# Optimization experiments

Hardware: AMD Instinct MI355X
Metric: run time of the kernel (lower is better)

## Reference

```python
import jax, jax.numpy as jnp
import numpy as np

EPS_RMS = 1e-8
EPS_Q = 1e-5


def rms_norm(x, scale):
    # full RMSNorm (p=-1): rms = ||x||_2 / sqrt(d); y = scale * x / (rms + eps)
    d = x.shape[-1]
    norm = jnp.linalg.norm(x, axis=-1, keepdims=True)
    rms = norm * (d ** -0.5)
    return scale * (x / (rms + EPS_RMS))


def activation_quant(x):
    # per-token int8 abs-max quant
    s = 127.0 / jnp.clip(jnp.max(jnp.abs(x), axis=-1, keepdims=True), EPS_Q, None)
    return jnp.clip(jnp.round(x * s), -128, 127) / s


def weight_quant(w):
    # per-tensor ternary abs-mean quant
    s = 1.0 / jnp.clip(jnp.mean(jnp.abs(w)), EPS_Q, None)
    return jnp.clip(jnp.round(w * s), -1, 1) / s


def bit_linear(x, w, scale):
    x_q = activation_quant(rms_norm(x, scale))  # forward value of STE
    w_q = weight_quant(w)
    return x_q @ w_q.T


def setup_inputs() -> dict:
    key = jax.random.key(0)
    ks = jax.random.split(key, 4)
    B = 65536
    x = jax.random.normal(ks[0], (B, 784), dtype=jnp.float32)
    w1 = jax.random.normal(ks[1], (128, 784), dtype=jnp.float32) * (784 ** -0.5)
    w2 = jax.random.normal(ks[2], (64, 128), dtype=jnp.float32) * (128 ** -0.5)
    w3 = jax.random.normal(ks[3], (10, 64), dtype=jnp.float32) * (64 ** -0.5)
    return {
        'x': x,
        'w1': w1, 'scale1': jnp.ones((784,), jnp.float32),
        'w2': w2, 'scale2': jnp.ones((128,), jnp.float32),
        'w3': w3, 'scale3': jnp.ones((64,), jnp.float32),
    }


def reference(x, w1, scale1, w2, scale2, w3, scale3):
    h = jax.nn.relu(bit_linear(x, w1, scale1))
    h = jax.nn.relu(bit_linear(h, w2, scale2))
    return bit_linear(h, w3, scale3)
```

## Files before the change

kernel.cpp:

```cpp
#include <hip/hip_runtime.h>
#include <stdint.h>


typedef int   ix4 __attribute__((ext_vector_type(4)));
typedef float fx4 __attribute__((ext_vector_type(4)));

#define MFMA_I8(a, b, c) __builtin_amdgcn_mfma_i32_16x16x64_i8((a), (b), (c), 0, 0, 0)

__device__ __forceinline__ void sync_lds() {
  asm volatile("s_waitcnt lgkmcnt(0)" ::: "memory");
  __builtin_amdgcn_s_barrier();
}
__device__ __forceinline__ void wave_lds_fence() {
  asm volatile("s_waitcnt lgkmcnt(0)" ::: "memory");
}

__global__ __launch_bounds__(256) void prep_mean(
    const float* __restrict__ w1, const float* __restrict__ w2,
    const float* __restrict__ w3, double* __restrict__ sums) {
  __shared__ double red[256];
  const int b = blockIdx.x;
  const float* w; int n, nb, bb, which;
  if (b < 240)      { w = w1; n = 128 * 784; nb = 240; bb = b;       which = 0; }
  else if (b < 248) { w = w2; n = 64 * 128;  nb = 8;   bb = b - 240; which = 1; }
  else              { w = w3; n = 10 * 64;   nb = 1;   bb = 0;       which = 2; }
  double s = 0.0;
  for (int i = bb * 256 + (int)threadIdx.x; i < n; i += nb * 256)
    s += (double)fabsf(w[i]);
  red[threadIdx.x] = s;
  __syncthreads();
  for (int off = 128; off > 0; off >>= 1) {
    if ((int)threadIdx.x < off) red[threadIdx.x] += red[threadIdx.x + off];
    __syncthreads();
  }
  if (threadIdx.x == 0) atomicAdd(&sums[which], red[0]);
}

__global__ __launch_bounds__(256) void prep_quant(
    const float* __restrict__ w1, const float* __restrict__ w2,
    const float* __restrict__ w3, const double* __restrict__ sums,
    int8_t* __restrict__ t1, int8_t* __restrict__ t2,
    int8_t* __restrict__ t3p) {
  const int idx = blockIdx.x * 256 + (int)threadIdx.x;
  const float s1 = 1.0f / fmaxf((float)(sums[0] * (1.0 / (128.0 * 784.0))), 1e-5f);
  const float s2 = 1.0f / fmaxf((float)(sums[1] * (1.0 / (64.0 * 128.0))), 1e-5f);
  const float s3 = 1.0f / fmaxf((float)(sums[2] * (1.0 / (10.0 * 64.0))), 1e-5f);
  if (idx < 128 * 832) {
    const int n = idx / 832, k = idx - n * 832;
    float v = 0.f;
    if (k < 784) v = fminf(fmaxf(rintf(w1[n * 784 + k] * s1), -1.f), 1.f);
    t1[idx] = (int8_t)(int)v;
  } else if (idx < 128 * 832 + 64 * 128) {
    const int i = idx - 128 * 832;
    t2[i] = (int8_t)(int)fminf(fmaxf(rintf(w2[i] * s2), -1.f), 1.f);
  } else if (idx < 128 * 832 + 64 * 128 + 16 * 64) {
    const int i = idx - (128 * 832 + 64 * 128);
    const int n = i >> 6, p = i & 63;
    const int ch = (p >> 2) + 16 * (p & 3);
    float v = 0.f;
    if (n < 10) v = fminf(fmaxf(rintf(w3[n * 64 + ch] * s3), -1.f), 1.f);
    t3p[i] = (int8_t)(int)v;
  }
}

__global__ __launch_bounds__(256)
__attribute__((amdgpu_waves_per_eu(2, 4)))
void ffn_l1(
    const float* __restrict__ x,
    const float* __restrict__ sc1, const float* __restrict__ sc2,
    const int8_t* __restrict__ t1, const double* __restrict__ sums,
    int8_t* __restrict__ q2g, float* __restrict__ inv2g, int numTiles) {
  __shared__ int8_t q1[16 * 848];
  __shared__ float  h1[16 * 132];
  __shared__ float  inv1[16];

  const int tid = threadIdx.x;
  const int l   = tid & 63;
  const int wv  = tid >> 6;
  const int g   = l >> 4;
  const int sl  = l & 15;
  const int token = wv * 4 + g;

  const float m1 = fmaxf((float)(sums[0] * (1.0 / (128.0 * 784.0))), 1e-5f);

  if (tid < 192) {
    const int t = tid / 12, c = tid - (tid / 12) * 12;
    *reinterpret_cast<unsigned*>(&q1[t * 848 + 784 + c * 4]) = 0u;
  }

  fx4 xv[13];
  int tile = blockIdx.x;
  if (tile < numTiles) {
    const float* rowp = x + (size_t)(tile * 16 + token) * 784;
#pragma unroll
    for (int c = 0; c < 12; ++c)
      xv[c] = *reinterpret_cast<const fx4*>(rowp + (sl + 16 * c) * 4);
    if (sl < 4) xv[12] = *reinterpret_cast<const fx4*>(rowp + (sl + 192) * 4);
  }

  for (; tile < numTiles; tile += (int)gridDim.x) {
    float ss = 0.f, am = 0.f;
#pragma unroll
    for (int c = 0; c < 12; ++c) {
      fx4 v = xv[c];
      fx4 s4 = *reinterpret_cast<const fx4*>(sc1 + (sl + 16 * c) * 4);
      ss += v[0] * v[0] + v[1] * v[1] + v[2] * v[2] + v[3] * v[3];
      am = fmaxf(am, fmaxf(fmaxf(fabsf(v[0] * s4[0]), fabsf(v[1] * s4[1])),
                           fmaxf(fabsf(v[2] * s4[2]), fabsf(v[3] * s4[3]))));
    }
    if (sl < 4) {
      fx4 v = xv[12];
      fx4 s4 = *reinterpret_cast<const fx4*>(sc1 + (sl + 192) * 4);
      ss += v[0] * v[0] + v[1] * v[1] + v[2] * v[2] + v[3] * v[3];
      am = fmaxf(am, fmaxf(fmaxf(fabsf(v[0] * s4[0]), fabsf(v[1] * s4[1])),
                           fmaxf(fabsf(v[2] * s4[2]), fabsf(v[3] * s4[3]))));
    }
#pragma unroll
    for (int m = 1; m < 16; m <<= 1) {
      ss += __shfl_xor(ss, m, 64);
      am = fmaxf(am, __shfl_xor(am, m, 64));
    }
    const float denom = sqrtf(ss) * (1.0f / 28.0f) + 1e-8f;
    const float invd  = 1.0f / denom;
    const float cl    = fmaxf(am * invd, 1e-5f);
    const float gq    = (127.0f / cl) * invd;
    if (sl == 0) inv1[token] = cl * (1.0f / 127.0f);

#pragma unroll
    for (int c = 0; c < 12; ++c) {
      fx4 v = xv[c];
      fx4 s4 = *reinterpret_cast<const fx4*>(sc1 + (sl + 16 * c) * 4);
      int q0 = (int)fminf(fmaxf(rintf(v[0] * s4[0] * gq), -128.f), 127.f);
      int q1i = (int)fminf(fmaxf(rintf(v[1] * s4[1] * gq), -128.f), 127.f);
      int q2i = (int)fminf(fmaxf(rintf(v[2] * s4[2] * gq), -128.f), 127.f);
      int q3i = (int)fminf(fmaxf(rintf(v[3] * s4[3] * gq), -128.f), 127.f);
      unsigned p = (unsigned)(q0 & 255) | ((unsigned)(q1i & 255) << 8) |
                   ((unsigned)(q2i & 255) << 16) | ((unsigned)(q3i & 255) << 24);
      *reinterpret_cast<unsigned*>(&q1[token * 848 + (sl + 16 * c) * 4]) = p;
    }
    if (sl < 4) {
      fx4 v = xv[12];
      fx4 s4 = *reinterpret_cast<const fx4*>(sc1 + (sl + 192) * 4);
      int q0 = (int)fminf(fmaxf(rintf(v[0] * s4[0] * gq), -128.f), 127.f);
      int q1i = (int)fminf(fmaxf(rintf(v[1] * s4[1] * gq), -128.f), 127.f);
      int q2i = (int)fminf(fmaxf(rintf(v[2] * s4[2] * gq), -128.f), 127.f);
      int q3i = (int)fminf(fmaxf(rintf(v[3] * s4[3] * gq), -128.f), 127.f);
      unsigned p = (unsigned)(q0 & 255) | ((unsigned)(q1i & 255) << 8) |
                   ((unsigned)(q2i & 255) << 16) | ((unsigned)(q3i & 255) << 24);
      *reinterpret_cast<unsigned*>(&q1[token * 848 + (sl + 192) * 4]) = p;
    }

    {
      const int ntile = tile + (int)gridDim.x;
      if (ntile < numTiles) {
        const float* rowp = x + (size_t)(ntile * 16 + token) * 784;
#pragma unroll
        for (int c = 0; c < 12; ++c)
          xv[c] = *reinterpret_cast<const fx4*>(rowp + (sl + 16 * c) * 4);
        if (sl < 4) xv[12] = *reinterpret_cast<const fx4*>(rowp + (sl + 192) * 4);
      }
    }

    sync_lds();

    ix4 acc0 = {0, 0, 0, 0}, acc1 = {0, 0, 0, 0};
    {
      const int8_t* b0p = t1 + (wv * 32 + sl) * 832;
      const int8_t* b1p = b0p + 16 * 832;
#pragma unroll 4
      for (int kk = 0; kk < 13; ++kk) {
        const int k0 = kk * 64 + g * 16;
        ix4 a  = *reinterpret_cast<const ix4*>(&q1[sl * 848 + k0]);
        ix4 b0 = *reinterpret_cast<const ix4*>(b0p + k0);
        ix4 b1 = *reinterpret_cast<const ix4*>(b1p + k0);
        acc0 = MFMA_I8(a, b0, acc0);
        acc1 = MFMA_I8(a, b1, acc1);
      }
    }
#pragma unroll
    for (int r = 0; r < 4; ++r) {
      const int tr = g * 4 + r;
      const float s = inv1[tr] * m1;
      h1[tr * 132 + wv * 32 + sl]      = fmaxf((float)acc0[r] * s, 0.f);
      h1[tr * 132 + wv * 32 + 16 + sl] = fmaxf((float)acc1[r] * s, 0.f);
    }
    sync_lds();

    {
      fx4 v0 = *reinterpret_cast<const fx4*>(&h1[token * 132 + sl * 4]);
      fx4 v1 = *reinterpret_cast<const fx4*>(&h1[token * 132 + 64 + sl * 4]);
      fx4 s0 = *reinterpret_cast<const fx4*>(sc2 + sl * 4);
      fx4 s1 = *reinterpret_cast<const fx4*>(sc2 + 64 + sl * 4);
      float ss2 = v0[0]*v0[0] + v0[1]*v0[1] + v0[2]*v0[2] + v0[3]*v0[3]
                + v1[0]*v1[0] + v1[1]*v1[1] + v1[2]*v1[2] + v1[3]*v1[3];
      float am2 = fmaxf(fmaxf(fmaxf(fabsf(v0[0]*s0[0]), fabsf(v0[1]*s0[1])),
                              fmaxf(fabsf(v0[2]*s0[2]), fabsf(v0[3]*s0[3]))),
                        fmaxf(fmaxf(fabsf(v1[0]*s1[0]), fabsf(v1[1]*s1[1])),
                              fmaxf(fabsf(v1[2]*s1[2]), fabsf(v1[3]*s1[3]))));
#pragma unroll
      for (int m = 1; m < 16; m <<= 1) {
        ss2 += __shfl_xor(ss2, m, 64);
        am2 = fmaxf(am2, __shfl_xor(am2, m, 64));
      }
      const float den2 = sqrtf(ss2) * 0.08838834764831845f + 1e-8f;
      const float id2  = 1.0f / den2;
      const float cl2  = fmaxf(am2 * id2, 1e-5f);
      const float gq2  = (127.0f / cl2) * id2;
      const size_t tok = (size_t)tile * 16 + token;
      if (sl == 0) inv2g[tok] = cl2 * (1.0f / 127.0f);
      int a0 = (int)fminf(fmaxf(rintf(v0[0]*s0[0]*gq2), -128.f), 127.f);
      int a1 = (int)fminf(fmaxf(rintf(v0[1]*s0[1]*gq2), -128.f), 127.f);
      int a2 = (int)fminf(fmaxf(rintf(v0[2]*s0[2]*gq2), -128.f), 127.f);
      int a3 = (int)fminf(fmaxf(rintf(v0[3]*s0[3]*gq2), -128.f), 127.f);
      int b0 = (int)fminf(fmaxf(rintf(v1[0]*s1[0]*gq2), -128.f), 127.f);
      int b1 = (int)fminf(fmaxf(rintf(v1[1]*s1[1]*gq2), -128.f), 127.f);
      int b2 = (int)fminf(fmaxf(rintf(v1[2]*s1[2]*gq2), -128.f), 127.f);
      int b3 = (int)fminf(fmaxf(rintf(v1[3]*s1[3]*gq2), -128.f), 127.f);
      unsigned pa = (unsigned)(a0 & 255) | ((unsigned)(a1 & 255) << 8) |
                    ((unsigned)(a2 & 255) << 16) | ((unsigned)(a3 & 255) << 24);
      unsigned pb = (unsigned)(b0 & 255) | ((unsigned)(b1 & 255) << 8) |
                    ((unsigned)(b2 & 255) << 16) | ((unsigned)(b3 & 255) << 24);
      *reinterpret_cast<unsigned*>(q2g + tok * 128 + sl * 4)      = pa;
      *reinterpret_cast<unsigned*>(q2g + tok * 128 + 64 + sl * 4) = pb;
    }
  }
}

__global__ __launch_bounds__(256) void ffn_l23(
    const int8_t* __restrict__ q2g, const float* __restrict__ inv2g,
    const float* __restrict__ sc3,
    const int8_t* __restrict__ t2, const int8_t* __restrict__ t3p,
    const double* __restrict__ sums, float* __restrict__ out) {
  __shared__ int8_t wbuf[4][16 * 64];

  const int tid = threadIdx.x;
  const int l   = tid & 63;
  const int wv  = tid >> 6;
  const int g   = l >> 4;
  const int sl  = l & 15;
  const int wtok0 = (blockIdx.x * 4 + wv) * 16;

  const float m2 = fmaxf((float)(sums[1] * (1.0 / (64.0 * 128.0))), 1e-5f);
  const float m3 = fmaxf((float)(sums[2] * (1.0 / (10.0 * 64.0))), 1e-5f);

  ix4 a0 = *reinterpret_cast<const ix4*>(q2g + (size_t)(wtok0 + sl) * 128 + g * 16);
  ix4 a1 = *reinterpret_cast<const ix4*>(q2g + (size_t)(wtok0 + sl) * 128 + 64 + g * 16);
  fx4 i2 = *reinterpret_cast<const fx4*>(inv2g + wtok0 + 4 * g);

  ix4 acc[4];
#pragma unroll
  for (int nt = 0; nt < 4; ++nt) {
    ix4 c = {0, 0, 0, 0};
    const int8_t* bp = t2 + (nt * 16 + sl) * 128;
    c = MFMA_I8(a0, *reinterpret_cast<const ix4*>(bp + g * 16), c);
    c = MFMA_I8(a1, *reinterpret_cast<const ix4*>(bp + 64 + g * 16), c);
    acc[nt] = c;
  }

  float sc3v[4];
#pragma unroll
  for (int nt = 0; nt < 4; ++nt) sc3v[nt] = sc3[nt * 16 + sl];

  float h2v[4][4];
  float ss3[4] = {0.f, 0.f, 0.f, 0.f}, am3[4] = {0.f, 0.f, 0.f, 0.f};
#pragma unroll
  for (int nt = 0; nt < 4; ++nt)
#pragma unroll
    for (int r = 0; r < 4; ++r) {
      float h = fmaxf((float)acc[nt][r] * i2[r] * m2, 0.f);
      h2v[nt][r] = h;
      ss3[r] += h * h;
      am3[r] = fmaxf(am3[r], fabsf(h * sc3v[nt]));
    }
#pragma unroll
  for (int m = 1; m < 16; m <<= 1) {
#pragma unroll
    for (int r = 0; r < 4; ++r) {
      ss3[r] += __shfl_xor(ss3[r], m, 64);
      am3[r] = fmaxf(am3[r], __shfl_xor(am3[r], m, 64));
    }
  }
  float gq3[4], i3[4];
#pragma unroll
  for (int r = 0; r < 4; ++r) {
    const float den3 = sqrtf(ss3[r]) * 0.125f + 1e-8f;
    const float id3  = 1.0f / den3;
    const float cl3  = fmaxf(am3[r] * id3, 1e-5f);
    gq3[r] = (127.0f / cl3) * id3;
    i3[r]  = cl3 * (1.0f / 127.0f) * m3;
  }

#pragma unroll
  for (int r = 0; r < 4; ++r) {
    int c0 = (int)fminf(fmaxf(rintf(h2v[0][r] * sc3v[0] * gq3[r]), -128.f), 127.f);
    int c1 = (int)fminf(fmaxf(rintf(h2v[1][r] * sc3v[1] * gq3[r]), -128.f), 127.f);
    int c2 = (int)fminf(fmaxf(rintf(h2v[2][r] * sc3v[2] * gq3[r]), -128.f), 127.f);
    int c3 = (int)fminf(fmaxf(rintf(h2v[3][r] * sc3v[3] * gq3[r]), -128.f), 127.f);
    unsigned p = (unsigned)(c0 & 255) | ((unsigned)(c1 & 255) << 8) |
                 ((unsigned)(c2 & 255) << 16) | ((unsigned)(c3 & 255) << 24);
    *reinterpret_cast<unsigned*>(&wbuf[wv][(4 * g + r) * 64 + sl * 4]) = p;
  }
  wave_lds_fence();

  ix4 a3 = *reinterpret_cast<const ix4*>(&wbuf[wv][sl * 64 + g * 16]);
  ix4 b3 = *reinterpret_cast<const ix4*>(t3p + sl * 64 + g * 16);
  ix4 acc3 = {0, 0, 0, 0};
  acc3 = MFMA_I8(a3, b3, acc3);

  if (sl < 10) {
#pragma unroll
    for (int r = 0; r < 4; ++r)
      out[(size_t)(wtok0 + 4 * g + r) * 10 + sl] = (float)acc3[r] * i3[r];
  }
}

extern "C" void kernel_launch(void* const* d_in, const int* in_sizes, int n_in,
                              void* d_out, int out_size, void* d_ws, size_t ws_size,
                              hipStream_t stream) {
  const float* x  = (const float*)d_in[0];
  const float* w1 = (const float*)d_in[1];
  const float* s1 = (const float*)d_in[2];
  const float* w2 = (const float*)d_in[3];
  const float* s2 = (const float*)d_in[4];
  const float* w3 = (const float*)d_in[5];
  const float* s3 = (const float*)d_in[6];
  float* out = (float*)d_out;

  char* ws = (char*)d_ws;
  double* sums = (double*)ws;
  int8_t* t1   = (int8_t*)(ws + 1024);
  int8_t* t2   = (int8_t*)(ws + 107520);
  int8_t* t3p  = (int8_t*)(ws + 115712);
  float*  inv2 = (float*)(ws + 116736);
  int8_t* q2   = (int8_t*)(ws + 378880);

  const int B = in_sizes[0] / 784;
  const int numTiles = B / 16;

  hipMemsetAsync(sums, 0, 3 * sizeof(double), stream);
  prep_mean<<<249, 256, 0, stream>>>(w1, w2, w3, sums);
  const int total_q = 128 * 832 + 64 * 128 + 16 * 64;
  prep_quant<<<(total_q + 255) / 256, 256, 0, stream>>>(w1, w2, w3, sums, t1, t2, t3p);
  const int grid1 = numTiles < 1024 ? numTiles : 1024;
  ffn_l1<<<grid1, 256, 0, stream>>>(x, s1, s2, t1, sums, q2, inv2, numTiles);
  ffn_l23<<<B / 64, 256, 0, stream>>>(q2, inv2, s3, t2, t3p, sums, out);
}
```

Before: 318.4 us.

## Fuse layers two and three into the first-layer kernel, dropping global intermediates

Merges the second and third BitLinear layers into the persistent layer-1 kernel. Wave 0 of each block quantizes h1 directly into MFMA operand registers and runs the remaining matmuls and quantization. This removes the global q2/inv2 intermediate write and reread and one kernel launch. In exchange, the other three waves sit idle during this per-tile tail, which lengthens each tile's critical path.

```diff
diff --git a/kernel.cpp b/kernel.cpp
--- a/kernel.cpp
+++ b/kernel.cpp
@@ -65,14 +65,17 @@
 
 __global__ __launch_bounds__(256)
 __attribute__((amdgpu_waves_per_eu(2, 4)))
-void ffn_l1(
+void ffn_fused(
     const float* __restrict__ x,
     const float* __restrict__ sc1, const float* __restrict__ sc2,
-    const int8_t* __restrict__ t1, const double* __restrict__ sums,
-    int8_t* __restrict__ q2g, float* __restrict__ inv2g, int numTiles) {
+    const float* __restrict__ sc3,
+    const int8_t* __restrict__ t1, const int8_t* __restrict__ t2,
+    const int8_t* __restrict__ t3p, const double* __restrict__ sums,
+    float* __restrict__ out, int numTiles) {
   __shared__ int8_t q1[16 * 848];
   __shared__ float  h1[16 * 132];
   __shared__ float  inv1[16];
+  __shared__ int8_t wbuf[16 * 64];
 
   const int tid = threadIdx.x;
   const int l   = tid & 63;
@@ -82,6 +85,8 @@
   const int token = wv * 4 + g;
 
   const float m1 = fmaxf((float)(sums[0] * (1.0 / (128.0 * 784.0))), 1e-5f);
+  const float m2 = fmaxf((float)(sums[1] * (1.0 / (64.0 * 128.0))), 1e-5f);
+  const float m3 = fmaxf((float)(sums[2] * (1.0 / (10.0 * 64.0))), 1e-5f);
 
   if (tid < 192) {
     const int t = tid / 12, c = tid - (tid / 12) * 12;
@@ -186,131 +191,118 @@
     }
     sync_lds();
 
-    {
-      fx4 v0 = *reinterpret_cast<const fx4*>(&h1[token * 132 + sl * 4]);
-      fx4 v1 = *reinterpret_cast<const fx4*>(&h1[token * 132 + 64 + sl * 4]);
-      fx4 s0 = *reinterpret_cast<const fx4*>(sc2 + sl * 4);
-      fx4 s1 = *reinterpret_cast<const fx4*>(sc2 + 64 + sl * 4);
-      float ss2 = v0[0]*v0[0] + v0[1]*v0[1] + v0[2]*v0[2] + v0[3]*v0[3]
-                + v1[0]*v1[0] + v1[1]*v1[1] + v1[2]*v1[2] + v1[3]*v1[3];
-      float am2 = fmaxf(fmaxf(fmaxf(fabsf(v0[0]*s0[0]), fabsf(v0[1]*s0[1])),
-                              fmaxf(fabsf(v0[2]*s0[2]), fabsf(v0[3]*s0[3]))),
-                        fmaxf(fmaxf(fabsf(v1[0]*s1[0]), fabsf(v1[1]*s1[1])),
-                              fmaxf(fabsf(v1[2]*s1[2]), fabsf(v1[3]*s1[3]))));
-#pragma unroll
-      for (int m = 1; m < 16; m <<= 1) {
-        ss2 += __shfl_xor(ss2, m, 64);
-        am2 = fmaxf(am2, __shfl_xor(am2, m, 64));
-      }
+    if (wv == 0) {
+      const float* hrow = &h1[sl * 132];
+      float ss2 = 0.f, am2 = 0.f;
+#pragma unroll
+      for (int half = 0; half < 2; ++half) {
+        const int base = half * 64 + g * 16;
+#pragma unroll
+        for (int q = 0; q < 4; ++q) {
+          fx4 v  = *reinterpret_cast<const fx4*>(hrow + base + q * 4);
+          fx4 s4 = *reinterpret_cast<const fx4*>(sc2 + base + q * 4);
+          ss2 += v[0]*v[0] + v[1]*v[1] + v[2]*v[2] + v[3]*v[3];
+          am2 = fmaxf(am2, fmaxf(fmaxf(fabsf(v[0]*s4[0]), fabsf(v[1]*s4[1])),
+                                 fmaxf(fabsf(v[2]*s4[2]), fabsf(v[3]*s4[3]))));
+        }
+      }
+      ss2 += __shfl_xor(ss2, 16, 64);
+      am2 = fmaxf(am2, __shfl_xor(am2, 16, 64));
+      ss2 += __shfl_xor(ss2, 32, 64);
+      am2 = fmaxf(am2, __shfl_xor(am2, 32, 64));
       const float den2 = sqrtf(ss2) * 0.08838834764831845f + 1e-8f;
       const float id2  = 1.0f / den2;
       const float cl2  = fmaxf(am2 * id2, 1e-5f);
       const float gq2  = (127.0f / cl2) * id2;
-      const size_t tok = (size_t)tile * 16 + token;
-      if (sl == 0) inv2g[tok] = cl2 * (1.0f / 127.0f);
-      int a0 = (int)fminf(fmaxf(rintf(v0[0]*s0[0]*gq2), -128.f), 127.f);
-      int a1 = (int)fminf(fmaxf(rintf(v0[1]*s0[1]*gq2), -128.f), 127.f);
-      int a2 = (int)fminf(fmaxf(rintf(v0[2]*s0[2]*gq2), -128.f), 127.f);
-      int a3 = (int)fminf(fmaxf(rintf(v0[3]*s0[3]*gq2), -128.f), 127.f);
-      int b0 = (int)fminf(fmaxf(rintf(v1[0]*s1[0]*gq2), -128.f), 127.f);
-      int b1 = (int)fminf(fmaxf(rintf(v1[1]*s1[1]*gq2), -128.f), 127.f);
-      int b2 = (int)fminf(fmaxf(rintf(v1[2]*s1[2]*gq2), -128.f), 127.f);
-      int b3 = (int)fminf(fmaxf(rintf(v1[3]*s1[3]*gq2), -128.f), 127.f);
-      unsigned pa = (unsigned)(a0 & 255) | ((unsigned)(a1 & 255) << 8) |
-                    ((unsigned)(a2 & 255) << 16) | ((unsigned)(a3 & 255) << 24);
-      unsigned pb = (unsigned)(b0 & 255) | ((unsigned)(b1 & 255) << 8) |
-                    ((unsigned)(b2 & 255) << 16) | ((unsigned)(b3 & 255) << 24);
-      *reinterpret_cast<unsigned*>(q2g + tok * 128 + sl * 4)      = pa;
-      *reinterpret_cast<unsigned*>(q2g + tok * 128 + 64 + sl * 4) = pb;
-    }
-  }
-}
-
-__global__ __launch_bounds__(256) void ffn_l23(
-    const int8_t* __restrict__ q2g, const float* __restrict__ inv2g,
-    const float* __restrict__ sc3,
-    const int8_t* __restrict__ t2, const int8_t* __restrict__ t3p,
-    const double* __restrict__ sums, float* __restrict__ out) {
-  __shared__ int8_t wbuf[4][16 * 64];
-
-  const int tid = threadIdx.x;
-  const int l   = tid & 63;
-  const int wv  = tid >> 6;
-  const int g   = l >> 4;
-  const int sl  = l & 15;
-  const int wtok0 = (blockIdx.x * 4 + wv) * 16;
-
-  const float m2 = fmaxf((float)(sums[1] * (1.0 / (64.0 * 128.0))), 1e-5f);
-  const float m3 = fmaxf((float)(sums[2] * (1.0 / (10.0 * 64.0))), 1e-5f);
-
-  ix4 a0 = *reinterpret_cast<const ix4*>(q2g + (size_t)(wtok0 + sl) * 128 + g * 16);
-  ix4 a1 = *reinterpret_cast<const ix4*>(q2g + (size_t)(wtok0 + sl) * 128 + 64 + g * 16);
-  fx4 i2 = *reinterpret_cast<const fx4*>(inv2g + wtok0 + 4 * g);
-
-  ix4 acc[4];
-#pragma unroll
-  for (int nt = 0; nt < 4; ++nt) {
-    ix4 c = {0, 0, 0, 0};
-    const int8_t* bp = t2 + (nt * 16 + sl) * 128;
-    c = MFMA_I8(a0, *reinterpret_cast<const ix4*>(bp + g * 16), c);
-    c = MFMA_I8(a1, *reinterpret_cast<const ix4*>(bp + 64 + g * 16), c);
-    acc[nt] = c;
-  }
-
-  float sc3v[4];
-#pragma unroll
-  for (int nt = 0; nt < 4; ++nt) sc3v[nt] = sc3[nt * 16 + sl];
-
-  float h2v[4][4];
-  float ss3[4] = {0.f, 0.f, 0.f, 0.f}, am3[4] = {0.f, 0.f, 0.f, 0.f};
-#pragma unroll
-  for (int nt = 0; nt < 4; ++nt)
-#pragma unroll
-    for (int r = 0; r < 4; ++r) {
-      float h = fmaxf((float)acc[nt][r] * i2[r] * m2, 0.f);
-      h2v[nt][r] = h;
-      ss3[r] += h * h;
-      am3[r] = fmaxf(am3[r], fabsf(h * sc3v[nt]));
-    }
-#pragma unroll
-  for (int m = 1; m < 16; m <<= 1) {
-#pragma unroll
-    for (int r = 0; r < 4; ++r) {
-      ss3[r] += __shfl_xor(ss3[r], m, 64);
-      am3[r] = fmaxf(am3[r], __shfl_xor(am3[r], m, 64));
-    }
-  }
-  float gq3[4], i3[4];
-#pragma unroll
-  for (int r = 0; r < 4; ++r) {
-    const float den3 = sqrtf(ss3[r]) * 0.125f + 1e-8f;
-    const float id3  = 1.0f / den3;
-    const float cl3  = fmaxf(am3[r] * id3, 1e-5f);
-    gq3[r] = (127.0f / cl3) * id3;
-    i3[r]  = cl3 * (1.0f / 127.0f) * m3;
-  }
-
-#pragma unroll
-  for (int r = 0; r < 4; ++r) {
-    int c0 = (int)fminf(fmaxf(rintf(h2v[0][r] * sc3v[0] * gq3[r]), -128.f), 127.f);
-    int c1 = (int)fminf(fmaxf(rintf(h2v[1][r] * sc3v[1] * gq3[r]), -128.f), 127.f);
-    int c2 = (int)fminf(fmaxf(rintf(h2v[2][r] * sc3v[2] * gq3[r]), -128.f), 127.f);
-    int c3 = (int)fminf(fmaxf(rintf(h2v[3][r] * sc3v[3] * gq3[r]), -128.f), 127.f);
-    unsigned p = (unsigned)(c0 & 255) | ((unsigned)(c1 & 255) << 8) |
-                 ((unsigned)(c2 & 255) << 16) | ((unsigned)(c3 & 255) << 24);
-    *reinterpret_cast<unsigned*>(&wbuf[wv][(4 * g + r) * 64 + sl * 4]) = p;
-  }
-  wave_lds_fence();
-
-  ix4 a3 = *reinterpret_cast<const ix4*>(&wbuf[wv][sl * 64 + g * 16]);
-  ix4 b3 = *reinterpret_cast<const ix4*>(t3p + sl * 64 + g * 16);
-  ix4 acc3 = {0, 0, 0, 0};
-  acc3 = MFMA_I8(a3, b3, acc3);
-
-  if (sl < 10) {
-#pragma unroll
-    for (int r = 0; r < 4; ++r)
-      out[(size_t)(wtok0 + 4 * g + r) * 10 + sl] = (float)acc3[r] * i3[r];
+      const float i2self = cl2 * (1.0f / 127.0f);
+
+      ix4 a2f[2];
+#pragma unroll
+      for (int half = 0; half < 2; ++half) {
+        const int base = half * 64 + g * 16;
+#pragma unroll
+        for (int q = 0; q < 4; ++q) {
+          fx4 v  = *reinterpret_cast<const fx4*>(hrow + base + q * 4);
+          fx4 s4 = *reinterpret_cast<const fx4*>(sc2 + base + q * 4);
+          int c0 = (int)fminf(fmaxf(rintf(v[0] * s4[0] * gq2), -128.f), 127.f);
+          int c1 = (int)fminf(fmaxf(rintf(v[1] * s4[1] * gq2), -128.f), 127.f);
+          int c2 = (int)fminf(fmaxf(rintf(v[2] * s4[2] * gq2), -128.f), 127.f);
+          int c3 = (int)fminf(fmaxf(rintf(v[3] * s4[3] * gq2), -128.f), 127.f);
+          a2f[half][q] = (int)((unsigned)(c0 & 255) | ((unsigned)(c1 & 255) << 8) |
+                               ((unsigned)(c2 & 255) << 16) | ((unsigned)(c3 & 255) << 24));
+        }
+      }
+
+      ix4 acc[4];
+#pragma unroll
+      for (int nt = 0; nt < 4; ++nt) {
+        const int8_t* bp = t2 + (nt * 16 + sl) * 128 + g * 16;
+        ix4 c = {0, 0, 0, 0};
+        c = MFMA_I8(a2f[0], *reinterpret_cast<const ix4*>(bp), c);
+        c = MFMA_I8(a2f[1], *reinterpret_cast<const ix4*>(bp + 64), c);
+        acc[nt] = c;
+      }
+
+      float i2tok[4];
+#pragma unroll
+      for (int r = 0; r < 4; ++r) i2tok[r] = __shfl(i2self, 4 * g + r, 64);
+
+      float sc3v[4];
+#pragma unroll
+      for (int nt = 0; nt < 4; ++nt) sc3v[nt] = sc3[nt * 16 + sl];
+
+      float h2v[4][4];
+      float ss3[4] = {0.f, 0.f, 0.f, 0.f}, am3[4] = {0.f, 0.f, 0.f, 0.f};
+#pragma unroll
+      for (int nt = 0; nt < 4; ++nt)
+#pragma unroll
+        for (int r = 0; r < 4; ++r) {
+          float h = fmaxf((float)acc[nt][r] * i2tok[r] * m2, 0.f);
+          h2v[nt][r] = h;
+          ss3[r] += h * h;
+          am3[r] = fmaxf(am3[r], fabsf(h * sc3v[nt]));
+        }
+#pragma unroll
+      for (int m = 1; m < 16; m <<= 1) {
+#pragma unroll
+        for (int r = 0; r < 4; ++r) {
+          ss3[r] += __shfl_xor(ss3[r], m, 64);
+          am3[r] = fmaxf(am3[r], __shfl_xor(am3[r], m, 64));
+        }
+      }
+      float gq3[4], i3[4];
+#pragma unroll
+      for (int r = 0; r < 4; ++r) {
+        const float den3 = sqrtf(ss3[r]) * 0.125f + 1e-8f;
+        const float id3  = 1.0f / den3;
+        const float cl3  = fmaxf(am3[r] * id3, 1e-5f);
+        gq3[r] = (127.0f / cl3) * id3;
+        i3[r]  = cl3 * (1.0f / 127.0f) * m3;
+      }
+
+#pragma unroll
+      for (int r = 0; r < 4; ++r) {
+        int c0 = (int)fminf(fmaxf(rintf(h2v[0][r] * sc3v[0] * gq3[r]), -128.f), 127.f);
+        int c1 = (int)fminf(fmaxf(rintf(h2v[1][r] * sc3v[1] * gq3[r]), -128.f), 127.f);
+        int c2 = (int)fminf(fmaxf(rintf(h2v[2][r] * sc3v[2] * gq3[r]), -128.f), 127.f);
+        int c3 = (int)fminf(fmaxf(rintf(h2v[3][r] * sc3v[3] * gq3[r]), -128.f), 127.f);
+        unsigned p = (unsigned)(c0 & 255) | ((unsigned)(c1 & 255) << 8) |
+                     ((unsigned)(c2 & 255) << 16) | ((unsigned)(c3 & 255) << 24);
+        *reinterpret_cast<unsigned*>(&wbuf[(4 * g + r) * 64 + sl * 4]) = p;
+      }
+      wave_lds_fence();
+
+      ix4 a3 = *reinterpret_cast<const ix4*>(&wbuf[sl * 64 + g * 16]);
+      ix4 b3 = *reinterpret_cast<const ix4*>(t3p + sl * 64 + g * 16);
+      ix4 acc3 = {0, 0, 0, 0};
+      acc3 = MFMA_I8(a3, b3, acc3);
+
+      if (sl < 10) {
+#pragma unroll
+        for (int r = 0; r < 4; ++r)
+          out[(size_t)(tile * 16 + 4 * g + r) * 10 + sl] = (float)acc3[r] * i3[r];
+      }
+    }
   }
 }
 
@@ -331,8 +323,6 @@
   int8_t* t1   = (int8_t*)(ws + 1024);
   int8_t* t2   = (int8_t*)(ws + 107520);
   int8_t* t3p  = (int8_t*)(ws + 115712);
-  float*  inv2 = (float*)(ws + 116736);
-  int8_t* q2   = (int8_t*)(ws + 378880);
 
   const int B = in_sizes[0] / 784;
   const int numTiles = B / 16;
@@ -342,6 +332,5 @@
   const int total_q = 128 * 832 + 64 * 128 + 16 * 64;
   prep_quant<<<(total_q + 255) / 256, 256, 0, stream>>>(w1, w2, w3, sums, t1, t2, t3p);
   const int grid1 = numTiles < 1024 ? numTiles : 1024;
-  ffn_l1<<<grid1, 256, 0, stream>>>(x, s1, s2, t1, sums, q2, inv2, numTiles);
-  ffn_l23<<<B / 64, 256, 0, stream>>>(q2, inv2, s3, t2, t3p, sums, out);
-}
+  ffn_fused<<<grid1, 256, 0, stream>>>(x, s1, s2, s3, t1, t2, t3p, sums, out, numTiles);
+}
```

Result: slower. 330.2 us (+3.7%).
